# Performance work log

Measured on AMD Instinct MI355X. Metric: run time of the kernel, lower is better.

## Reference

```python
import jax, jax.numpy as jnp
import numpy as np

EPS = 1e-5
H = W = 14  # spatial grid, N = H*W = 196


def layernorm(x, g, b):
    m = x.mean(-1, keepdims=True)
    v = ((x - m) ** 2).mean(-1, keepdims=True)
    return (x - m) * jax.lax.rsqrt(v + EPS) * g + b


def fem_step(x, s):
    # x: [B, C, H, W]; blockwise instance-norm -> sigmoid gate -> 0.5*x + 0.5*attn*x
    B, C, h, w = x.shape
    nbh = -(-h // s)
    nbw = -(-w // s)
    idh = np.arange(h) // s
    idw = np.arange(w) // s
    bid_np = (idh[:, None] * nbw + idw[None, :]).reshape(-1)  # [h*w]
    cnt = jnp.asarray(np.bincount(bid_np, minlength=nbh * nbw).astype(np.float32))
    bid = jnp.asarray(bid_np)
    xt = x.reshape(B, C, h * w).transpose(2, 0, 1)  # [HW, B, C]
    s1 = jax.ops.segment_sum(xt, bid, num_segments=nbh * nbw)      # [nblk, B, C]
    s2 = jax.ops.segment_sum(xt * xt, bid, num_segments=nbh * nbw)
    mean = s1 / cnt[:, None, None]
    var = s2 / cnt[:, None, None] - mean * mean  # biased var, as F.instance_norm
    attn = jax.nn.sigmoid((xt - mean[bid]) * jax.lax.rsqrt(var[bid] + EPS))
    out = 0.5 * xt * (1.0 + attn)  # 0.5*x + 0.5*attn*x
    return out.transpose(1, 2, 0).reshape(B, C, h, w)


def fem(x):
    # p=[2,1,0] -> block sizes H//4=3, H//2=7, H//1=14
    for s in (H // 4, H // 2, H):
        x = fem_step(x, s)
    return x


def setup_inputs() -> dict:
    key = jax.random.key(0)
    ks = jax.random.split(key, 4)
    B, N, C = 64, H * W, 1024
    hid = 4 * C
    return {
        "x": jax.random.normal(ks[0], (B, N, C), jnp.float32),
        "ln1_g": jnp.ones((C,), jnp.float32),
        "ln1_b": jnp.zeros((C,), jnp.float32),
        "cw": jax.random.normal(ks[1], (H, W // 2 + 1, C, 2), jnp.float32) * 0.02,
        "ln2_g": jnp.ones((C,), jnp.float32),
        "ln2_b": jnp.zeros((C,), jnp.float32),
        "fc1_w": jax.random.normal(ks[2], (C, hid), jnp.float32) * 0.02,
        "fc1_b": jnp.zeros((hid,), jnp.float32),
        "fc2_w": jax.random.normal(ks[3], (hid, C), jnp.float32) * 0.02,
        "fc2_b": jnp.zeros((C,), jnp.float32),
    }


def reference(x, ln1_g, ln1_b, cw, ln2_g, ln2_b, fc1_w, fc1_b, fc2_w, fc2_b):
    B, N, C = x.shape
    # FFT global filter
    y = layernorm(x, ln1_g, ln1_b)
    yf = jnp.fft.rfft2(y.reshape(B, H, W, C), axes=(1, 2), norm="ortho")
    yf = yf * (cw[..., 0] + 1j * cw[..., 1])
    y = jnp.fft.irfft2(yf, s=(H, W), axes=(1, 2), norm="ortho").reshape(B, N, C)
    # MLP
    y = layernorm(y, ln2_g, ln2_b)
    y = jax.nn.gelu(y @ fc1_w + fc1_b, approximate=False) @ fc2_w + fc2_b
    # FEM on [B, C, H, W]
    y = fem(y.transpose(0, 2, 1).reshape(B, C, H, W))
    y = y.reshape(B, C, N).transpose(0, 2, 1)
    return x + y
```

## Files before the change

### kernel.cpp

```cpp
#include <hip/hip_runtime.h>

constexpr int CB = 64;
constexpr int CHH = 14, CWW = 14;
constexpr int CN = 196;
constexpr int CC = 1024;
constexpr int CROWS = CB * CN;
constexpr int CKW = 8;

constexpr float C14[14] = {
  1.0f, 0.9009688679024191f, 0.6234898018587336f, 0.2225209339563144f,
  -0.2225209339563144f, -0.6234898018587336f, -0.9009688679024191f, -1.0f,
  -0.9009688679024191f, -0.6234898018587336f, -0.2225209339563144f,
  0.2225209339563144f, 0.6234898018587336f, 0.9009688679024191f };
constexpr float S14[14] = {
  0.0f, 0.4338837391175581f, 0.7818314824680298f, 0.9749279121818236f,
  0.9749279121818236f, 0.7818314824680298f, 0.4338837391175581f, 0.0f,
  -0.4338837391175581f, -0.7818314824680298f, -0.9749279121818236f,
  -0.9749279121818236f, -0.7818314824680298f, -0.4338837391175581f };

typedef __attribute__((ext_vector_type(8))) short bf16x8;
typedef __attribute__((ext_vector_type(4))) float f32x4;

__device__ __forceinline__ unsigned short f2bf(float f) {
  unsigned u = __builtin_bit_cast(unsigned, f);
  u += 0x7FFFu + ((u >> 16) & 1u);
  return (unsigned short)(u >> 16);
}
__device__ __forceinline__ float bf2f(unsigned short h) {
  return __builtin_bit_cast(float, (unsigned)h << 16);
}

__device__ __forceinline__ void gload_lds16(const void* g, void* l) {
  __builtin_amdgcn_global_load_lds(
      (const __attribute__((address_space(1))) void*)g,
      (__attribute__((address_space(3))) void*)l, 16, 0, 0);
}

#define WAITV(N)  asm volatile("s_waitcnt vmcnt(" #N ")" ::: "memory")
#define SBAR()    asm volatile("s_barrier" ::: "memory")

template<int OUTBF>
__global__ __launch_bounds__(256)
void ln_kernel(const float* __restrict__ in, const float* __restrict__ gam,
               const float* __restrict__ bet, float* __restrict__ outf,
               unsigned short* __restrict__ outb)
{
  const int row = blockIdx.x;
  const int t = threadIdx.x;
  const float4 v = *(const float4*)(in + (size_t)row * CC + t * 4);
  float s  = v.x + v.y + v.z + v.w;
  float s2 = v.x*v.x + v.y*v.y + v.z*v.z + v.w*v.w;
  #pragma unroll
  for (int o = 32; o > 0; o >>= 1) { s += __shfl_down(s, o); s2 += __shfl_down(s2, o); }
  __shared__ float red[8];
  const int wid = t >> 6, lane = t & 63;
  if (lane == 0) { red[wid] = s; red[4 + wid] = s2; }
  __syncthreads();
  s  = red[0] + red[1] + red[2] + red[3];
  s2 = red[4] + red[5] + red[6] + red[7];
  const float mean = s * (1.0f / CC);
  const float var  = s2 * (1.0f / CC) - mean * mean;
  const float r = rsqrtf(var + 1e-5f);
  const float4 g4 = *(const float4*)(gam + t * 4);
  const float4 b4 = *(const float4*)(bet + t * 4);
  const float o0 = (v.x - mean) * r * g4.x + b4.x;
  const float o1 = (v.y - mean) * r * g4.y + b4.y;
  const float o2 = (v.z - mean) * r * g4.z + b4.z;
  const float o3 = (v.w - mean) * r * g4.w + b4.w;
  if (OUTBF) {
    ushort4 p; p.x = f2bf(o0); p.y = f2bf(o1); p.z = f2bf(o2); p.w = f2bf(o3);
    *(ushort4*)(outb + (size_t)row * CC + t * 4) = p;
  } else {
    *(float4*)(outf + (size_t)row * CC + t * 4) = make_float4(o0, o1, o2, o3);
  }
}

__global__ __launch_bounds__(256)
void fft_w_fwd(const float* __restrict__ y, float* __restrict__ Ar, float* __restrict__ Ai)
{
  const int t = threadIdx.x;
  const int bid = blockIdx.x;
  const int cc = bid & 3;
  const int tmp = bid >> 2;
  const int h = tmp % 14;
  const int b = tmp / 14;
  const int c = cc * 256 + t;
  const size_t base = ((size_t)b * CN + (size_t)h * CWW) * CC + c;
  float v[14];
  #pragma unroll
  for (int w = 0; w < 14; w++) v[w] = y[base + (size_t)w * CC];
  const size_t obase = (((size_t)b * CHH + h) * CKW) * CC + c;
  #pragma unroll
  for (int kw = 0; kw < 8; kw++) {
    float sr = 0.f, si = 0.f;
    #pragma unroll
    for (int w = 0; w < 14; w++) {
      const int m = (w * kw) % 14;
      sr += v[w] * C14[m];
      si -= v[w] * S14[m];
    }
    Ar[obase + (size_t)kw * CC] = sr;
    Ai[obase + (size_t)kw * CC] = si;
  }
}

__global__ __launch_bounds__(256)
void fft_h_filt(const float* __restrict__ Ar, const float* __restrict__ Ai,
                const float* __restrict__ cw, float* __restrict__ Br, float* __restrict__ Bi)
{
  const int t = threadIdx.x;
  const int bid = blockIdx.x;
  const int cc = bid & 3;
  const int tmp = bid >> 2;
  const int kw = tmp & 7;
  const int b = tmp >> 3;
  const int c = cc * 256 + t;
  const size_t base = (((size_t)b * CHH) * CKW + kw) * CC + c;
  float ar[14], ai[14];
  #pragma unroll
  for (int h = 0; h < 14; h++) {
    ar[h] = Ar[base + (size_t)h * (CKW * CC)];
    ai[h] = Ai[base + (size_t)h * (CKW * CC)];
  }
  float fr[14], fi[14];
  #pragma unroll
  for (int kh = 0; kh < 14; kh++) {
    float yr = 0.f, yi = 0.f;
    #pragma unroll
    for (int h = 0; h < 14; h++) {
      const int m = (h * kh) % 14;
      yr += ar[h] * C14[m] + ai[h] * S14[m];
      yi += ai[h] * C14[m] - ar[h] * S14[m];
    }
    const size_t widx = (((size_t)kh * CKW + kw) * CC + c) * 2;
    const float wr = cw[widx], wi = cw[widx + 1];
    fr[kh] = yr * wr - yi * wi;
    fi[kh] = yr * wi + yi * wr;
  }
  #pragma unroll
  for (int h = 0; h < 14; h++) {
    float sr = 0.f, si = 0.f;
    #pragma unroll
    for (int kh = 0; kh < 14; kh++) {
      const int m = (h * kh) % 14;
      sr += fr[kh] * C14[m] - fi[kh] * S14[m];
      si += fr[kh] * S14[m] + fi[kh] * C14[m];
    }
    Br[base + (size_t)h * (CKW * CC)] = sr;
    Bi[base + (size_t)h * (CKW * CC)] = si;
  }
}

__global__ __launch_bounds__(256)
void fft_w_inv(const float* __restrict__ Br, const float* __restrict__ Bi, float* __restrict__ y2)
{
  const int t = threadIdx.x;
  const int bid = blockIdx.x;
  const int cc = bid & 3;
  const int tmp = bid >> 2;
  const int h = tmp % 14;
  const int b = tmp / 14;
  const int c = cc * 256 + t;
  const size_t ibase = (((size_t)b * CHH + h) * CKW) * CC + c;
  float br[8], bi[8];
  #pragma unroll
  for (int k = 0; k < 8; k++) {
    br[k] = Br[ibase + (size_t)k * CC];
    bi[k] = Bi[ibase + (size_t)k * CC];
  }
  const size_t obase = ((size_t)b * CN + (size_t)h * CWW) * CC + c;
  #pragma unroll
  for (int w = 0; w < 14; w++) {
    float s = br[0] + ((w & 1) ? -br[7] : br[7]);
    #pragma unroll
    for (int k = 1; k < 7; k++) {
      const int m = (w * k) % 14;
      s += 2.0f * (br[k] * C14[m] - bi[k] * S14[m]);
    }
    y2[obase + (size_t)w * CC] = s * (1.0f / 196.0f);
  }
}

__global__ __launch_bounds__(256)
void transpose_f32_bf16(const float* __restrict__ in, unsigned short* __restrict__ out,
                        int R, int Ccols)
{
  __shared__ float tile[32][33];
  const int tx = threadIdx.x & 31;
  const int ty = threadIdx.x >> 5;
  const int cb = blockIdx.x * 32;
  const int rb = blockIdx.y * 32;
  #pragma unroll
  for (int i = 0; i < 32; i += 8)
    tile[ty + i][tx] = in[(size_t)(rb + ty + i) * Ccols + cb + tx];
  __syncthreads();
  #pragma unroll
  for (int i = 0; i < 32; i += 8)
    out[(size_t)(cb + ty + i) * R + rb + tx] = f2bf(tile[tx][ty + i]);
}

#define STAGE(REG, TILE_, DST) do {                                           \
  const unsigned short* _g = (((REG) < 2) ? A : BT);                          \
  const int _gb = (((REG) < 2) ? brow : bcol);                                \
  int _r0, _r1;                                                               \
  if ((REG) == 0)      { _r0 = vA;       _r1 = 128 + vA; }                    \
  else if ((REG) == 1) { _r0 = 64 + vA;  _r1 = 192 + vA; }                    \
  else if ((REG) == 2) { _r0 = ((vA>>5)<<6) + (vA&31);      _r1 = _r0 + 128; }\
  else                 { _r0 = ((vA>>5)<<6) + 32 + (vA&31); _r1 = _r0 + 128; }\
  const int _gc = (TILE_) * 64 + cl;                                          \
  gload_lds16(_g + (size_t)(_gb + _r0) * K + _gc, (DST) + _r0 * 128 + dcol16);\
  gload_lds16(_g + (size_t)(_gb + _r1) * K + _gc, (DST) + _r1 * 128 + dcol16);\
} while (0)

#define LOADA(CAarr, MH) do {                                                 \
  _Pragma("unroll")                                                           \
  for (int mf = 0; mf < 4; ++mf) {                                            \
    const int row = wm * 128 + (MH) * 64 + mf * 16 + lrow;                    \
    const int sw = (row & 7) << 4;                                            \
    af[mf][0] = *(const bf16x8*)((CAarr) + row * 128 + ((0  | dq) ^ sw));     \
    af[mf][1] = *(const bf16x8*)((CAarr) + row * 128 + ((64 | dq) ^ sw));     \
  }                                                                           \
} while (0)

#define LOADB(CBarr, DEST, NH) do {                                           \
  _Pragma("unroll")                                                           \
  for (int nf = 0; nf < 2; ++nf) {                                            \
    const int row = wn * 64 + ((NH) * 2 + nf) * 16 + lrow;                    \
    const int sw = (row & 7) << 4;                                            \
    DEST[nf][0] = *(const bf16x8*)((CBarr) + row * 128 + ((0  | dq) ^ sw));   \
    DEST[nf][1] = *(const bf16x8*)((CBarr) + row * 128 + ((64 | dq) ^ sw));   \
  }                                                                           \
} while (0)

#define MFMA8(MH, NH, BFR) do {                                               \
  _Pragma("unroll")                                                           \
  for (int ks = 0; ks < 2; ++ks)                                              \
    _Pragma("unroll")                                                         \
    for (int mf = 0; mf < 4; ++mf)                                            \
      _Pragma("unroll")                                                       \
      for (int nf = 0; nf < 2; ++nf)                                          \
        acc[(MH) * 4 + mf][(NH) * 2 + nf] = __builtin_amdgcn_mfma_f32_16x16x32_bf16( \
            af[mf][ks], BFR[nf][ks], acc[(MH) * 4 + mf][(NH) * 2 + nf], 0, 0, 0); \
} while (0)

#define TILEBODY(TT, CAarr, CBarr, NAarr, NBarr) do {                         \
  WAITV(0);                                                                   \
  SBAR();                                                                     \
  if ((TT) + 1 < NT) {                                                        \
    STAGE(0, (TT)+1, NAarr);                                                  \
    STAGE(2, (TT)+1, NBarr);                                                  \
    STAGE(3, (TT)+1, NBarr);                                                  \
    STAGE(1, (TT)+1, NAarr);                                                  \
  }                                                                           \
  LOADB(CBarr, bf0, 0);                                                       \
  LOADB(CBarr, bf1, 1);                                                       \
  LOADA(CAarr, 0);                                                            \
  MFMA8(0, 0, bf0);                                                           \
  MFMA8(0, 1, bf1);                                                           \
  LOADA(CAarr, 1);                                                            \
  MFMA8(1, 0, bf0);                                                           \
  MFMA8(1, 1, bf1);                                                           \
} while (0)

template<int DO_GELU>
__global__ __launch_bounds__(512, 2)
void gemm256(const unsigned short* __restrict__ A, const unsigned short* __restrict__ BT,
             const float* __restrict__ bias, unsigned short* __restrict__ C,
             int M, int N, int K)
{
  __shared__ __align__(16) short A0s[256 * 64];
  __shared__ __align__(16) short A1s[256 * 64];
  __shared__ __align__(16) short B0s[256 * 64];
  __shared__ __align__(16) short B1s[256 * 64];
  char* a0 = (char*)A0s; char* a1 = (char*)A1s;
  char* b0 = (char*)B0s; char* b1 = (char*)B1s;

  const int t = threadIdx.x;
  const int wid = t >> 6, lane = t & 63;
  const int wm = wid >> 2, wn = wid & 3;
  const int lrow = lane & 15, qk = lane >> 4;
  const int dq = qk << 4;

  const int nbx = N >> 8, nby = M >> 8;
  const int nwg = nbx * nby;
  const int orig = blockIdx.x;
  const int q8 = nwg >> 3, r8 = nwg & 7, xcd = orig & 7, lid = orig >> 3;
  const int wg = (xcd < r8 ? xcd * (q8 + 1) : r8 * (q8 + 1) + (xcd - r8) * q8) + lid;
  const int gw = 4 * nby;
  const int gid = wg / gw, rem = wg % gw;
  const int bx = gid * 4 + (rem & 3);
  const int by = rem >> 2;
  const int brow = by << 8, bcol = bx << 8;
  const int NT = K >> 6;

  const int vA = t >> 3;
  const int cl = ((t ^ (t >> 3)) & 7) << 3;
  const int dcol16 = (t & 7) << 4;

  f32x4 acc[8][4] = {};
  bf16x8 af[4][2], bf0[2][2], bf1[2][2];

  STAGE(0, 0, a0); STAGE(2, 0, b0); STAGE(3, 0, b0); STAGE(1, 0, a0);

  for (int T = 0; T < NT; T += 2) {
    TILEBODY(T,     a0, b0, a1, b1);
    TILEBODY(T + 1, a1, b1, a0, b0);
  }

  #pragma unroll
  for (int mf = 0; mf < 8; ++mf) {
    #pragma unroll
    for (int nf = 0; nf < 4; ++nf) {
      const int ccol = bcol + wn * 64 + nf * 16 + lrow;
      const float bb = bias[ccol];
      #pragma unroll
      for (int j = 0; j < 4; ++j) {
        const int r = brow + wm * 128 + mf * 16 + qk * 4 + j;
        float v = acc[mf][nf][j] + bb;
        if (DO_GELU) v = 0.5f * v * (1.0f + erff(v * 0.70710678118654752f));
        C[(size_t)r * N + ccol] = f2bf(v);
      }
    }
  }
}

__device__ __forceinline__ void fem_block(unsigned short* col, int t,
                                          int h0, int nh, int w0, int nw)
{
  float s = 0.f, s2 = 0.f;
  for (int ih = 0; ih < nh; ih++)
    for (int iw = 0; iw < nw; iw++) {
      const float v = bf2f(col[((h0 + ih) * 14 + w0 + iw) * 128 + t]);
      s += v; s2 += v * v;
    }
  const float inv = 1.0f / (float)(nh * nw);
  const float m = s * inv;
  const float var = s2 * inv - m * m;
  const float r = rsqrtf(var + 1e-5f);
  for (int ih = 0; ih < nh; ih++)
    for (int iw = 0; iw < nw; iw++) {
      const int idx = ((h0 + ih) * 14 + w0 + iw) * 128 + t;
      const float v = bf2f(col[idx]);
      const float a = 1.0f / (1.0f + __expf(-(v - m) * r));
      col[idx] = f2bf(0.5f * v * (1.0f + a));
    }
}

__global__ __launch_bounds__(128)
void fem_kernel(const unsigned short* __restrict__ z, const float* __restrict__ x,
                float* __restrict__ out)
{
  __shared__ unsigned short buf[CN * 128];
  const int t = threadIdx.x;
  const int b = blockIdx.x >> 3;
  const int cc = blockIdx.x & 7;
  const int c = cc * 128 + t;
  const size_t base = (size_t)b * CN * CC + c;
  #pragma unroll 4
  for (int n = 0; n < CN; n++) buf[n * 128 + t] = z[base + (size_t)n * CC];
  const int st3[5] = {0, 3, 6, 9, 12};
  const int ln3[5] = {3, 3, 3, 3, 2};
  for (int i = 0; i < 5; i++)
    for (int j = 0; j < 5; j++)
      fem_block(buf, t, st3[i], ln3[i], st3[j], ln3[j]);
  for (int i = 0; i < 2; i++)
    for (int j = 0; j < 2; j++)
      fem_block(buf, t, i * 7, 7, j * 7, 7);
  fem_block(buf, t, 0, 14, 0, 14);
  #pragma unroll 4
  for (int n = 0; n < CN; n++)
    out[base + (size_t)n * CC] = x[base + (size_t)n * CC] + bf2f(buf[n * 128 + t]);
}

extern "C" void kernel_launch(void* const* d_in, const int* in_sizes, int n_in,
                              void* d_out, int out_size, void* d_ws, size_t ws_size,
                              hipStream_t stream) {
  const float* x     = (const float*)d_in[0];
  const float* ln1_g = (const float*)d_in[1];
  const float* ln1_b = (const float*)d_in[2];
  const float* cw    = (const float*)d_in[3];
  const float* ln2_g = (const float*)d_in[4];
  const float* ln2_b = (const float*)d_in[5];
  const float* fc1_w = (const float*)d_in[6];
  const float* fc1_b = (const float*)d_in[7];
  const float* fc2_w = (const float*)d_in[8];
  const float* fc2_b = (const float*)d_in[9];
  float* out = (float*)d_out;
  char* ws = (char*)d_ws;

  const size_t SZ_A = (size_t)CB * CHH * CKW * CC * 4;
  float* Ar = (float*)(ws);
  float* Ai = (float*)(ws + SZ_A);
  float* Br = (float*)(ws + 2 * SZ_A);
  float* Bi = (float*)(ws + 3 * SZ_A);
  unsigned short* A1   = (unsigned short*)(ws);
  unsigned short* W1T  = (unsigned short*)(ws + SZ_A);
  unsigned short* W2T  = (unsigned short*)(ws + SZ_A + (size_t)4096 * 1024 * 2);
  unsigned short* Hmid = (unsigned short*)(ws + 2 * SZ_A);
  unsigned short* Z    = (unsigned short*)(ws);

  ln_kernel<0><<<CROWS, 256, 0, stream>>>(x, ln1_g, ln1_b, out, nullptr);
  fft_w_fwd<<<CB * CHH * 4, 256, 0, stream>>>(out, Ar, Ai);
  fft_h_filt<<<CB * CKW * 4, 256, 0, stream>>>(Ar, Ai, cw, Br, Bi);
  fft_w_inv<<<CB * CHH * 4, 256, 0, stream>>>(Br, Bi, out);
  ln_kernel<1><<<CROWS, 256, 0, stream>>>(out, ln2_g, ln2_b, nullptr, A1);
  transpose_f32_bf16<<<dim3(4096 / 32, 1024 / 32), 256, 0, stream>>>(fc1_w, W1T, 1024, 4096);
  transpose_f32_bf16<<<dim3(1024 / 32, 4096 / 32), 256, 0, stream>>>(fc2_w, W2T, 4096, 1024);
  gemm256<1><<<dim3(784), 512, 0, stream>>>(A1, W1T, fc1_b, Hmid, CROWS, 4096, 1024);
  gemm256<0><<<dim3(196), 512, 0, stream>>>(Hmid, W2T, fc2_b, Z, CROWS, 1024, 4096);
  fem_kernel<<<CB * 8, 128, 0, stream>>>(Z, x, out);
}
```

Before: 501.8 us.

## Replace 256x256 GEMM with 128x128 tiles loading B directly to registers

```diff
diff --git a/kernel.cpp b/kernel.cpp
--- a/kernel.cpp
+++ b/kernel.cpp
@@ -199,123 +199,106 @@
     out[(size_t)(cb + ty + i) * R + rb + tx] = f2bf(tile[tx][ty + i]);
 }
 
-#define STAGE(REG, TILE_, DST) do {                                           \
-  const unsigned short* _g = (((REG) < 2) ? A : BT);                          \
-  const int _gb = (((REG) < 2) ? brow : bcol);                                \
-  int _r0, _r1;                                                               \
-  if ((REG) == 0)      { _r0 = vA;       _r1 = 128 + vA; }                    \
-  else if ((REG) == 1) { _r0 = 64 + vA;  _r1 = 192 + vA; }                    \
-  else if ((REG) == 2) { _r0 = ((vA>>5)<<6) + (vA&31);      _r1 = _r0 + 128; }\
-  else                 { _r0 = ((vA>>5)<<6) + 32 + (vA&31); _r1 = _r0 + 128; }\
-  const int _gc = (TILE_) * 64 + cl;                                          \
-  gload_lds16(_g + (size_t)(_gb + _r0) * K + _gc, (DST) + _r0 * 128 + dcol16);\
-  gload_lds16(_g + (size_t)(_gb + _r1) * K + _gc, (DST) + _r1 * 128 + dcol16);\
-} while (0)
-
-#define LOADA(CAarr, MH) do {                                                 \
+#define TILE128(TT, CUR, NXT, BCUR, BNXT) do {                                \
+  WAITV(8);                                                                   \
+  SBAR();                                                                     \
+  if ((TT) + 1 < NT) {                                                        \
+    const int _gc = ((TT) + 1) * 64 + cl;                                     \
+    gload_lds16(A + (size_t)(brow + ar0     ) * K + _gc, (NXT) + dst0);       \
+    gload_lds16(A + (size_t)(brow + ar0 + 32) * K + _gc, (NXT) + dst0 + 4096);\
+    gload_lds16(A + (size_t)(brow + ar0 + 64) * K + _gc, (NXT) + dst0 + 8192);\
+    gload_lds16(A + (size_t)(brow + ar0 + 96) * K + _gc, (NXT) + dst0 + 12288);\
+    _Pragma("unroll")                                                         \
+    for (int nf = 0; nf < 4; ++nf) {                                          \
+      const size_t _b = (size_t)(bcol + wn * 64 + nf * 16 + lrow) * K         \
+                        + ((TT) + 1) * 64 + qe;                               \
+      BNXT[nf][0] = *(const bf16x8*)(BT + _b);                                \
+      BNXT[nf][1] = *(const bf16x8*)(BT + _b + 32);                           \
+    }                                                                         \
+  }                                                                           \
   _Pragma("unroll")                                                           \
   for (int mf = 0; mf < 4; ++mf) {                                            \
-    const int row = wm * 128 + (MH) * 64 + mf * 16 + lrow;                    \
+    const int row = wm * 64 + mf * 16 + lrow;                                 \
     const int sw = (row & 7) << 4;                                            \
-    af[mf][0] = *(const bf16x8*)((CAarr) + row * 128 + ((0  | dq) ^ sw));     \
-    af[mf][1] = *(const bf16x8*)((CAarr) + row * 128 + ((64 | dq) ^ sw));     \
+    af[mf][0] = *(const bf16x8*)((CUR) + row * 128 + ((0  | dq) ^ sw));       \
+    af[mf][1] = *(const bf16x8*)((CUR) + row * 128 + ((64 | dq) ^ sw));       \
   }                                                                           \
-} while (0)
-
-#define LOADB(CBarr, DEST, NH) do {                                           \
-  _Pragma("unroll")                                                           \
-  for (int nf = 0; nf < 2; ++nf) {                                            \
-    const int row = wn * 64 + ((NH) * 2 + nf) * 16 + lrow;                    \
-    const int sw = (row & 7) << 4;                                            \
-    DEST[nf][0] = *(const bf16x8*)((CBarr) + row * 128 + ((0  | dq) ^ sw));   \
-    DEST[nf][1] = *(const bf16x8*)((CBarr) + row * 128 + ((64 | dq) ^ sw));   \
-  }                                                                           \
-} while (0)
-
-#define MFMA8(MH, NH, BFR) do {                                               \
+  if ((TT) + 1 < NT) { WAITV(12); } else { WAITV(0); }                        \
+  __builtin_amdgcn_s_setprio(1);                                              \
   _Pragma("unroll")                                                           \
   for (int ks = 0; ks < 2; ++ks)                                              \
     _Pragma("unroll")                                                         \
     for (int mf = 0; mf < 4; ++mf)                                            \
       _Pragma("unroll")                                                       \
-      for (int nf = 0; nf < 2; ++nf)                                          \
-        acc[(MH) * 4 + mf][(NH) * 2 + nf] = __builtin_amdgcn_mfma_f32_16x16x32_bf16( \
-            af[mf][ks], BFR[nf][ks], acc[(MH) * 4 + mf][(NH) * 2 + nf], 0, 0, 0); \
+      for (int nf = 0; nf < 4; ++nf)                                          \
+        acc[mf][nf] = __builtin_amdgcn_mfma_f32_16x16x32_bf16(                \
+            af[mf][ks], BCUR[nf][ks], acc[mf][nf], 0, 0, 0);                  \
+  __builtin_amdgcn_s_setprio(0);                                              \
 } while (0)
 
-#define TILEBODY(TT, CAarr, CBarr, NAarr, NBarr) do {                         \
-  WAITV(0);                                                                   \
-  SBAR();                                                                     \
-  if ((TT) + 1 < NT) {                                                        \
-    STAGE(0, (TT)+1, NAarr);                                                  \
-    STAGE(2, (TT)+1, NBarr);                                                  \
-    STAGE(3, (TT)+1, NBarr);                                                  \
-    STAGE(1, (TT)+1, NAarr);                                                  \
-  }                                                                           \
-  LOADB(CBarr, bf0, 0);                                                       \
-  LOADB(CBarr, bf1, 1);                                                       \
-  LOADA(CAarr, 0);                                                            \
-  MFMA8(0, 0, bf0);                                                           \
-  MFMA8(0, 1, bf1);                                                           \
-  LOADA(CAarr, 1);                                                            \
-  MFMA8(1, 0, bf0);                                                           \
-  MFMA8(1, 1, bf1);                                                           \
-} while (0)
-
 template<int DO_GELU>
-__global__ __launch_bounds__(512, 2)
-void gemm256(const unsigned short* __restrict__ A, const unsigned short* __restrict__ BT,
+__global__ __launch_bounds__(256, 2)
+void gemm128(const unsigned short* __restrict__ A, const unsigned short* __restrict__ BT,
              const float* __restrict__ bias, unsigned short* __restrict__ C,
              int M, int N, int K)
 {
-  __shared__ __align__(16) short A0s[256 * 64];
-  __shared__ __align__(16) short A1s[256 * 64];
-  __shared__ __align__(16) short B0s[256 * 64];
-  __shared__ __align__(16) short B1s[256 * 64];
-  char* a0 = (char*)A0s; char* a1 = (char*)A1s;
-  char* b0 = (char*)B0s; char* b1 = (char*)B1s;
+  __shared__ __align__(16) short As0[128 * 64];
+  __shared__ __align__(16) short As1[128 * 64];
+  char* a0 = (char*)As0; char* a1 = (char*)As1;
 
   const int t = threadIdx.x;
   const int wid = t >> 6, lane = t & 63;
-  const int wm = wid >> 2, wn = wid & 3;
+  const int wm = wid >> 1, wn = wid & 1;
   const int lrow = lane & 15, qk = lane >> 4;
   const int dq = qk << 4;
-
-  const int nbx = N >> 8, nby = M >> 8;
+  const int qe = qk << 3;
+
+  const int nbx = N >> 7, nby = M >> 7;
   const int nwg = nbx * nby;
   const int orig = blockIdx.x;
-  const int q8 = nwg >> 3, r8 = nwg & 7, xcd = orig & 7, lid = orig >> 3;
-  const int wg = (xcd < r8 ? xcd * (q8 + 1) : r8 * (q8 + 1) + (xcd - r8) * q8) + lid;
-  const int gw = 4 * nby;
+  const int q8 = nwg >> 3, xcd = orig & 7, lid = orig >> 3;
+  const int wg = xcd * q8 + lid;
+  const int gw = 8 * nby;
   const int gid = wg / gw, rem = wg % gw;
-  const int bx = gid * 4 + (rem & 3);
-  const int by = rem >> 2;
-  const int brow = by << 8, bcol = bx << 8;
+  const int bx = gid * 8 + (rem & 7);
+  const int by = rem >> 3;
+  const int brow = by << 7, bcol = bx << 7;
   const int NT = K >> 6;
 
-  const int vA = t >> 3;
+  const int ar0 = t >> 3;
   const int cl = ((t ^ (t >> 3)) & 7) << 3;
-  const int dcol16 = (t & 7) << 4;
-
-  f32x4 acc[8][4] = {};
-  bf16x8 af[4][2], bf0[2][2], bf1[2][2];
-
-  STAGE(0, 0, a0); STAGE(2, 0, b0); STAGE(3, 0, b0); STAGE(1, 0, a0);
+  const int dst0 = t * 16;
+
+  f32x4 acc[4][4] = {};
+  bf16x8 af[4][2], bfX[4][2], bfY[4][2];
+
+  {
+    gload_lds16(A + (size_t)(brow + ar0     ) * K + cl, a0 + dst0);
+    gload_lds16(A + (size_t)(brow + ar0 + 32) * K + cl, a0 + dst0 + 4096);
+    gload_lds16(A + (size_t)(brow + ar0 + 64) * K + cl, a0 + dst0 + 8192);
+    gload_lds16(A + (size_t)(brow + ar0 + 96) * K + cl, a0 + dst0 + 12288);
+    #pragma unroll
+    for (int nf = 0; nf < 4; ++nf) {
+      const size_t _b = (size_t)(bcol + wn * 64 + nf * 16 + lrow) * K + qe;
+      bfX[nf][0] = *(const bf16x8*)(BT + _b);
+      bfX[nf][1] = *(const bf16x8*)(BT + _b + 32);
+    }
+  }
 
   for (int T = 0; T < NT; T += 2) {
-    TILEBODY(T,     a0, b0, a1, b1);
-    TILEBODY(T + 1, a1, b1, a0, b0);
-  }
-
-  #pragma unroll
-  for (int mf = 0; mf < 8; ++mf) {
+    TILE128(T,     a0, a1, bfX, bfY);
+    TILE128(T + 1, a1, a0, bfY, bfX);
+  }
+
+  #pragma unroll
+  for (int mf = 0; mf < 4; ++mf) {
     #pragma unroll
     for (int nf = 0; nf < 4; ++nf) {
       const int ccol = bcol + wn * 64 + nf * 16 + lrow;
       const float bb = bias[ccol];
       #pragma unroll
       for (int j = 0; j < 4; ++j) {
-        const int r = brow + wm * 128 + mf * 16 + qk * 4 + j;
+        const int r = brow + wm * 64 + mf * 16 + qk * 4 + j;
         float v = acc[mf][nf][j] + bb;
         if (DO_GELU) v = 0.5f * v * (1.0f + erff(v * 0.70710678118654752f));
         C[(size_t)r * N + ccol] = f2bf(v);
@@ -406,7 +389,7 @@
   ln_kernel<1><<<CROWS, 256, 0, stream>>>(out, ln2_g, ln2_b, nullptr, A1);
   transpose_f32_bf16<<<dim3(4096 / 32, 1024 / 32), 256, 0, stream>>>(fc1_w, W1T, 1024, 4096);
   transpose_f32_bf16<<<dim3(1024 / 32, 4096 / 32), 256, 0, stream>>>(fc2_w, W2T, 4096, 1024);
-  gemm256<1><<<dim3(784), 512, 0, stream>>>(A1, W1T, fc1_b, Hmid, CROWS, 4096, 1024);
-  gemm256<0><<<dim3(196), 512, 0, stream>>>(Hmid, W2T, fc2_b, Z, CROWS, 1024, 4096);
+  gemm128<1><<<dim3(3136), 256, 0, stream>>>(A1, W1T, fc1_b, Hmid, CROWS, 4096, 1024);
+  gemm128<0><<<dim3(784), 256, 0, stream>>>(Hmid, W2T, fc2_b, Z, CROWS, 1024, 4096);
   fem_kernel<<<CB * 8, 128, 0, stream>>>(Z, x, out);
 }
```

Result: slower. 736.5 us (+46.8%).
